# Kernel tuning notes

Measured on AMD Instinct MI355X. Metric: run time of the kernel, lower is better.

## Reference

```python
import jax, jax.numpy as jnp
import numpy as np

B, ID, OD = 4096, 2048, 1024


def _conv_softmax(x, w):
    # x: [..., L]; torch Conv1d(1,1,k=3,stride=1,pad=1,bias=False) then softmax(dim=-1)
    L = x.shape[-1]
    xp = jnp.pad(x, [(0, 0)] * (x.ndim - 1) + [(1, 1)])
    y = w[0] * xp[..., 0:L] + w[1] * xp[..., 1:L + 1] + w[2] * xp[..., 2:L + 2]
    return jax.nn.softmax(y, axis=-1)


def _lstm_cell(x, h, c, Wih, Whh, bih, bhh):
    # torch LSTMCell gate order: i, f, g, o
    g = x @ Wih.T + h @ Whh.T + (bih + bhh)
    i, f, gg, o = jnp.split(g, 4, axis=-1)
    c2 = jax.nn.sigmoid(f) * c + jax.nn.sigmoid(i) * jnp.tanh(gg)
    h2 = jax.nn.sigmoid(o) * jnp.tanh(c2)
    return h2, c2


def _lstm_params(key, in_dim, hid):
    k = 1.0 / np.sqrt(hid)
    ks = jax.random.split(key, 4)
    Wih = jax.random.uniform(ks[0], (4 * hid, in_dim), jnp.float32, -k, k)
    Whh = jax.random.uniform(ks[1], (4 * hid, hid), jnp.float32, -k, k)
    bih = jax.random.uniform(ks[2], (4 * hid,), jnp.float32, -k, k)
    bhh = jax.random.uniform(ks[3], (4 * hid,), jnp.float32, -k, k)
    return Wih, Whh, bih, bhh


def setup_inputs() -> dict:
    key = jax.random.key(0)
    ks = jax.random.split(key, 12)
    spec = jax.random.normal(ks[0], (B, ID), jnp.float32)
    Wih1, Whh1, bih1, bhh1 = _lstm_params(ks[1], ID, OD)
    Wih2, Whh2, bih2, bhh2 = _lstm_params(ks[2], ID // 2, OD // 2)
    Wih3, Whh3, bih3, bhh3 = _lstm_params(ks[3], ID // 4, OD // 4)
    Wih4, Whh4, bih4, bhh4 = _lstm_params(ks[4], ID // 8, OD // 8)
    ck = np.sqrt(1.0 / 3.0)  # Conv1d(1,1,3) init bound
    w2_1h = jax.random.uniform(ks[5], (3,), jnp.float32, -ck, ck)
    w2_1c = jax.random.uniform(ks[6], (3,), jnp.float32, -ck, ck)
    w3_2h = jax.random.uniform(ks[7], (3,), jnp.float32, -ck, ck)
    w3_2c = jax.random.uniform(ks[8], (3,), jnp.float32, -ck, ck)
    w4_3h = jax.random.uniform(ks[9], (3,), jnp.float32, -ck, ck)
    w4_3c = jax.random.uniform(ks[10], (3,), jnp.float32, -ck, ck)
    return dict(spec=spec,
                Wih1=Wih1, Whh1=Whh1, bih1=bih1, bhh1=bhh1,
                Wih2=Wih2, Whh2=Whh2, bih2=bih2, bhh2=bhh2,
                Wih3=Wih3, Whh3=Whh3, bih3=bih3, bhh3=bhh3,
                Wih4=Wih4, Whh4=Whh4, bih4=bih4, bhh4=bhh4,
                w2_1h=w2_1h, w2_1c=w2_1c, w3_2h=w3_2h, w3_2c=w3_2c,
                w4_3h=w4_3h, w4_3c=w4_3c)


def reference(spec, Wih1, Whh1, bih1, bhh1, Wih2, Whh2, bih2, bhh2,
              Wih3, Whh3, bih3, bhh3, Wih4, Whh4, bih4, bhh4,
              w2_1h, w2_1c, w3_2h, w3_2c, w4_3h, w4_3c):
    b = spec.shape[0]
    # Level 4: 8 independent steps, fresh zero state each (torch code passes no hidden)
    x4 = spec.reshape(b, 8, ID // 8)
    z4 = jnp.zeros((b, 8, OD // 8), spec.dtype)
    h4, c4 = _lstm_cell(x4, z4, z4, Wih4, Whh4, bih4, bhh4)   # [b,8,OD/8]
    hb4 = _conv_softmax(h4.reshape(b, 4, OD // 4), w4_3h)      # pairs -> [b,4,OD/4]
    cb4 = _conv_softmax(c4.reshape(b, 4, OD // 4), w4_3c)
    # Level 3: 4 independent steps seeded by level-4 blended states
    x3 = spec.reshape(b, 4, ID // 4)
    h3, c3 = _lstm_cell(x3, hb4, cb4, Wih3, Whh3, bih3, bhh3)  # [b,4,OD/4]
    hb3 = _conv_softmax(h3.reshape(b, 2, OD // 2), w3_2h)      # [b,2,OD/2]
    cb3 = _conv_softmax(c3.reshape(b, 2, OD // 2), w3_2c)
    # Level 2: 2 independent steps
    x2 = spec.reshape(b, 2, ID // 2)
    h2, c2 = _lstm_cell(x2, hb3, cb3, Wih2, Whh2, bih2, bhh2)  # [b,2,OD/2]
    hb2 = _conv_softmax(h2.reshape(b, OD), w2_1h)              # [b,OD]
    cb2 = _conv_softmax(c2.reshape(b, OD), w2_1c)
    # Level 1: single full-resolution step; forward returns out1 = h1
    h1, c1 = _lstm_cell(spec, hb2, cb2, Wih1, Whh1, bih1, bhh1)
    return h1
```

## Files before the change

kernel.cpp:

```cpp
#include <hip/hip_runtime.h>


typedef __bf16 bf16x8 __attribute__((ext_vector_type(8)));
typedef float f32x4 __attribute__((ext_vector_type(4)));
typedef unsigned short u16x4 __attribute__((ext_vector_type(4)));

#define AS1 __attribute__((address_space(1)))
#define AS3 __attribute__((address_space(3)))

__device__ __forceinline__ unsigned short f2bf(float f) {
    union { float f; unsigned int i; } v; v.f = f;
    unsigned int r = v.i + 0x7fffu + ((v.i >> 16) & 1u);
    return (unsigned short)(r >> 16);
}
__device__ __forceinline__ float bf2f(unsigned short u) {
    union { unsigned int i; float f; } v; v.i = ((unsigned int)u) << 16; return v.f;
}
__device__ __forceinline__ float sigm(float x) { return 1.f / (1.f + __expf(-x)); }
__device__ __forceinline__ float tanh_(float x) { float e = __expf(2.f * x); return 1.f - 2.f / (e + 1.f); }

__global__ __launch_bounds__(256) void cvt_spec3(
    const float* __restrict__ spec, unsigned short* __restrict__ sB,
    unsigned short* __restrict__ X, unsigned short* __restrict__ Y, long n4)
{
    const long stride = (long)gridDim.x * blockDim.x;
    for (long i = (long)blockIdx.x * blockDim.x + threadIdx.x; i < n4; i += stride) {
        const float4 v = ((const float4*)spec)[i];
        u16x4 o; o.x = f2bf(v.x); o.y = f2bf(v.y); o.z = f2bf(v.z); o.w = f2bf(v.w);
        ((u16x4*)sB)[i] = o;
        const long b = i >> 9;
        const int c4 = (int)(i & 511);
        *(u16x4*)(X + (b * 4 + (c4 >> 7)) * 768  + ((c4 & 127) << 2)) = o;
        *(u16x4*)(Y + (b * 2 + (c4 >> 8)) * 1536 + ((c4 & 255) << 2)) = o;
    }
}

__global__ __launch_bounds__(256) void cvt_specA(
    const float* __restrict__ spec, unsigned short* __restrict__ dst, long n4)
{
    const long stride = (long)gridDim.x * blockDim.x;
    for (long i = (long)blockIdx.x * blockDim.x + threadIdx.x; i < n4; i += stride) {
        const float4 v = ((const float4*)spec)[i];
        const long m = i >> 9;
        const int col = ((int)(i & 511)) << 2;
        u16x4 o; o.x = f2bf(v.x); o.y = f2bf(v.y); o.z = f2bf(v.z); o.w = f2bf(v.w);
        *(u16x4*)(dst + m * 3072 + col) = o;
    }
}

struct PSeg { const float* src; unsigned short* dst; long g0; int H; int kshift; int dstld; int dstcol; };
struct PArgs { PSeg s[7]; long total; };

__global__ __launch_bounds__(256) void cvt_permW_all(PArgs pa)
{
    const long stride = (long)gridDim.x * blockDim.x;
    for (long gi = (long)blockIdx.x * blockDim.x + threadIdx.x; gi < pa.total; gi += stride) {
        int si = 0;
#pragma unroll
        for (int k = 1; k < 7; ++k) si += (gi >= pa.s[k].g0);
        const PSeg sg = pa.s[si];
        const long i = gi - sg.g0;
        const int kq = 1 << sg.kshift;
        const int p = (int)(i >> sg.kshift);
        const int kk = ((int)i & (kq - 1)) << 2;
        const int o = ((p >> 6) << 4) | (p & 15);
        const int q = (p >> 4) & 3;
        const long r = (long)q * sg.H + o;
        const float4 v = *(const float4*)(sg.src + (r << (sg.kshift + 2)) + kk);
        u16x4 wv; wv.x = f2bf(v.x); wv.y = f2bf(v.y); wv.z = f2bf(v.z); wv.w = f2bf(v.w);
        *(u16x4*)(sg.dst + (long)p * sg.dstld + sg.dstcol + kk) = wv;
    }
}

__global__ __launch_bounds__(256) void bias_all(
    const float* __restrict__ bih1, const float* __restrict__ bhh1,
    const float* __restrict__ bih2, const float* __restrict__ bhh2,
    const float* __restrict__ bih3, const float* __restrict__ bhh3,
    const float* __restrict__ bih4, const float* __restrict__ bhh4,
    float* __restrict__ bs1, float* __restrict__ bs2,
    float* __restrict__ bs3, float* __restrict__ bs4)
{
    const int i = blockIdx.x * 256 + threadIdx.x;
    const float *bih, *bhh; float* dst; int H, j;
    if (i < 4096)      { bih = bih1; bhh = bhh1; dst = bs1; H = 1024; j = i; }
    else if (i < 6144) { bih = bih2; bhh = bhh2; dst = bs2; H = 512;  j = i - 4096; }
    else if (i < 7168) { bih = bih3; bhh = bhh3; dst = bs3; H = 256;  j = i - 6144; }
    else               { bih = bih4; bhh = bhh4; dst = bs4; H = 128;  j = i - 7168; }
    const int o = ((j >> 6) << 4) | (j & 15);
    const int q = (j >> 4) & 3;
    dst[j] = bih[q * H + o] + bhh[q * H + o];
}

#define QUAD(AF, S, NS, BF)                                                                 \
    { _Pragma("unroll") for (int mi = 0; mi < 4; ++mi) {                                    \
        _Pragma("unroll") for (int ni = 0; ni < 2; ++ni) {                                  \
            acc[(S)*4+mi][(NS)*2+ni] = __builtin_amdgcn_mfma_f32_16x16x32_bf16(             \
                AF[mi][0], BF[ni][0], acc[(S)*4+mi][(NS)*2+ni], 0, 0, 0);                   \
            acc[(S)*4+mi][(NS)*2+ni] = __builtin_amdgcn_mfma_f32_16x16x32_bf16(             \
                AF[mi][1], BF[ni][1], acc[(S)*4+mi][(NS)*2+ni], 0, 0, 0);                   \
    } } }

#define GLL(gsrc, loff) __builtin_amdgcn_global_load_lds(                                   \
    (const AS1 void*)(gsrc), (AS3 void*)(lds + (loff)), 16, 0, 0)

#define FENCE asm volatile("" ::: "memory")

template<bool HAS_CIN, bool LAST>
__global__ __launch_bounds__(512, 2) void gemm8(
    const unsigned short* __restrict__ A, const unsigned short* __restrict__ W, const int K,
    const float* __restrict__ bsum, const unsigned short* __restrict__ Cin,
    float* __restrict__ HoutF, unsigned short* __restrict__ HoutB,
    unsigned short* __restrict__ CoutB, const int H)
{
    __shared__ __align__(16) char lds[131072];
    const int t = threadIdx.x;
    const int w = t >> 6, l = t & 63;
    const int wr = w >> 2, wc = w & 3;

    const int GX = gridDim.x, GY = gridDim.y;
    const int nwg = GX * GY;
    const int bid = (int)blockIdx.y * GX + (int)blockIdx.x;
    const int swz = (bid & 7) * (nwg >> 3) + (bid >> 3);
    const int m0 = (swz / GY) * 256, n0 = (swz % GY) * 256;

    const int colsw = ((l & 7) ^ (l >> 3)) * 8;
    const size_t k128 = (size_t)128 * K;
    const size_t aoff0 = (size_t)(m0 + w * 16 + (l >> 3)) * K + colsw;
    const size_t aoff1 = aoff0 + (size_t)8 * K;
    const size_t boff0 = (size_t)(n0 + w * 16 + (l >> 3)) * K + colsw;
    const size_t boff1 = boff0 + (size_t)8 * K;
    const int sd0 = w * 2048 + l * 16;
    const int sd1 = sd0 + 1024;

    const int lr128 = (l & 15) * 128;
    const int sw0 = (((l >> 4)    ) ^ (l & 7)) * 16;
    const int sw1 = (((l >> 4) + 4) ^ (l & 7)) * 16;

    f32x4 acc[8][4];
#pragma unroll
    for (int i = 0; i < 8; ++i)
#pragma unroll
        for (int j = 0; j < 4; ++j) acc[i][j] = (f32x4){0.f, 0.f, 0.f, 0.f};

    const int NT = K >> 6;

    GLL(A + aoff0, sd0);                      GLL(A + aoff1, sd1);
    GLL(A + aoff0 + k128, 16384 + sd0);       GLL(A + aoff1 + k128, 16384 + sd1);
    GLL(W + boff0, 32768 + sd0);              GLL(W + boff1, 32768 + sd1);
    GLL(W + boff0 + k128, 49152 + sd0);       GLL(W + boff1 + k128, 49152 + sd1);
    GLL(W + boff0 + 64, 98304 + sd0);         GLL(W + boff1 + 64, 98304 + sd1);
    GLL(W + boff0 + k128 + 64, 114688 + sd0); GLL(W + boff1 + k128 + 64, 114688 + sd1);

    bf16x8 aLo[4][2], aHi[4][2], bF0[2][2], bF1[2][2];

    for (int tt = 0; tt < NT; ++tt) {
        const int q = tt & 1, qn = q ^ 1;
        const int rbA = (q << 16) + (wr << 14) + lr128;
        const int rbB = (q << 16) + 32768 + wc * 8192 + lr128;
        const bool st1 = (tt + 1 < NT), st2 = (tt + 2 < NT);

        if (st1) { asm volatile("s_waitcnt vmcnt(4)" ::: "memory"); }
        else     { asm volatile("s_waitcnt vmcnt(0)" ::: "memory"); }
        __builtin_amdgcn_s_barrier();
        FENCE;

#pragma unroll
        for (int mi = 0; mi < 4; ++mi) {
            aLo[mi][0] = *(const bf16x8*)(lds + rbA + mi * 2048 + sw0);
            aLo[mi][1] = *(const bf16x8*)(lds + rbA + mi * 2048 + sw1);
        }
#pragma unroll
        for (int ni = 0; ni < 2; ++ni) {
            bF0[ni][0] = *(const bf16x8*)(lds + rbB + ni * 2048 + sw0);
            bF0[ni][1] = *(const bf16x8*)(lds + rbB + ni * 2048 + sw1);
            bF1[ni][0] = *(const bf16x8*)(lds + rbB + 4096 + ni * 2048 + sw0);
            bF1[ni][1] = *(const bf16x8*)(lds + rbB + 4096 + ni * 2048 + sw1);
        }
        if (st1) {
            const size_t ko1 = (size_t)(tt + 1) * 64;
            GLL(A + aoff0 + ko1, (qn << 16) + sd0);
            GLL(A + aoff1 + ko1, (qn << 16) + sd1);
            GLL(A + aoff0 + k128 + ko1, (qn << 16) + 16384 + sd0);
            GLL(A + aoff1 + k128 + ko1, (qn << 16) + 16384 + sd1);
        }
#pragma unroll
        for (int mi = 0; mi < 4; ++mi) {
            aHi[mi][0] = *(const bf16x8*)(lds + rbA + 8192 + mi * 2048 + sw0);
            aHi[mi][1] = *(const bf16x8*)(lds + rbA + 8192 + mi * 2048 + sw1);
        }

        __builtin_amdgcn_s_setprio(1);
        QUAD(aLo, 0, 0, bF0);
        QUAD(aLo, 0, 1, bF1);
        __builtin_amdgcn_s_setprio(0);
        __builtin_amdgcn_s_barrier();
        FENCE;

        if (st2) {
            const size_t ko2 = (size_t)(tt + 2) * 64;
            GLL(W + boff0 + ko2, (q << 16) + 32768 + sd0);
            GLL(W + boff1 + ko2, (q << 16) + 32768 + sd1);
            GLL(W + boff0 + k128 + ko2, (q << 16) + 49152 + sd0);
            GLL(W + boff1 + k128 + ko2, (q << 16) + 49152 + sd1);
        }
        __builtin_amdgcn_s_setprio(1);
        QUAD(aHi, 1, 1, bF1);
        QUAD(aHi, 1, 0, bF0);
        __builtin_amdgcn_s_setprio(0);
    }

    const int ocol = (n0 >> 6) * 16 + wc * 16 + (l & 15);
    const int bb = n0 + wc * 64 + (l & 15);
    const float b0 = bsum[bb], b1 = bsum[bb + 16], b2 = bsum[bb + 32], b3 = bsum[bb + 48];
    const int mrow0 = m0 + wr * 128 + (l >> 4) * 4;
#pragma unroll
    for (int mi = 0; mi < 8; ++mi)
#pragma unroll
        for (int j = 0; j < 4; ++j) {
            const size_t m = (size_t)(mrow0 + mi * 16 + j);
            const float gi = acc[mi][0][j] + b0;
            const float gf = acc[mi][1][j] + b1;
            const float gg = acc[mi][2][j] + b2;
            const float go = acc[mi][3][j] + b3;
            float c2 = sigm(gi) * tanh_(gg);
            if (HAS_CIN) c2 += sigm(gf) * bf2f(Cin[m * H + ocol]);
            const float h2 = sigm(go) * tanh_(c2);
            if (LAST) {
                HoutF[m * H + ocol] = h2;
            } else {
                HoutB[m * H + ocol] = f2bf(h2);
                CoutB[m * H + ocol] = f2bf(c2);
            }
        }
}

template<int L>
__global__ __launch_bounds__(256) void conv_dual(
    const unsigned short* __restrict__ Hin, const unsigned short* __restrict__ Cin,
    const float* __restrict__ w3h, const float* __restrict__ w3c,
    unsigned short* __restrict__ Yb, int ldYb, unsigned short* __restrict__ cbuf)
{
    __shared__ float xs[L + 2];
    __shared__ float red[8];
    const int nrows = gridDim.x >> 1;
    const bool isC = (int)blockIdx.x >= nrows;
    const int row = isC ? ((int)blockIdx.x - nrows) : (int)blockIdx.x;
    const unsigned short* Xs = isC ? Cin : Hin;
    const float* w3 = isC ? w3c : w3h;
    const int t = threadIdx.x;
    const size_t base = (size_t)row * L;
    const float w0 = w3[0], w1 = w3[1], w2 = w3[2];
    if (t == 0) { xs[0] = 0.f; xs[L + 1] = 0.f; }
    for (int i = t; i < L; i += 256) xs[i + 1] = bf2f(Xs[base + i]);
    __syncthreads();
    constexpr int E = L / 256;
    float y[E];
    float vmax = -3.4e38f;
#pragma unroll
    for (int i = 0; i < E; ++i) {
        const int c = t + i * 256;
        y[i] = w0 * xs[c] + w1 * xs[c + 1] + w2 * xs[c + 2];
        vmax = fmaxf(vmax, y[i]);
    }
#pragma unroll
    for (int off = 32; off >= 1; off >>= 1) vmax = fmaxf(vmax, __shfl_xor(vmax, off));
    if ((t & 63) == 0) red[t >> 6] = vmax;
    __syncthreads();
    vmax = fmaxf(fmaxf(red[0], red[1]), fmaxf(red[2], red[3]));
    float s = 0.f;
#pragma unroll
    for (int i = 0; i < E; ++i) { y[i] = __expf(y[i] - vmax); s += y[i]; }
#pragma unroll
    for (int off = 32; off >= 1; off >>= 1) s += __shfl_xor(s, off);
    if ((t & 63) == 0) red[4 + (t >> 6)] = s;
    __syncthreads();
    const float inv = 1.f / (red[4] + red[5] + red[6] + red[7]);
#pragma unroll
    for (int i = 0; i < E; ++i) {
        const int c = t + i * 256;
        const float v = y[i] * inv;
        if (isC) cbuf[base + c] = f2bf(v);
        else     Yb[(size_t)row * ldYb + c] = f2bf(v);
    }
}

extern "C" void kernel_launch(void* const* d_in, const int* in_sizes, int n_in,
                              void* d_out, int out_size, void* d_ws, size_t ws_size,
                              hipStream_t stream)
{
    (void)in_sizes; (void)n_in; (void)out_size; (void)ws_size;
    const float* spec  = (const float*)d_in[0];
    const float* Wih1  = (const float*)d_in[1];
    const float* Whh1  = (const float*)d_in[2];
    const float* bih1  = (const float*)d_in[3];
    const float* bhh1  = (const float*)d_in[4];
    const float* Wih2  = (const float*)d_in[5];
    const float* Whh2  = (const float*)d_in[6];
    const float* bih2  = (const float*)d_in[7];
    const float* bhh2  = (const float*)d_in[8];
    const float* Wih3  = (const float*)d_in[9];
    const float* Whh3  = (const float*)d_in[10];
    const float* bih3  = (const float*)d_in[11];
    const float* bhh3  = (const float*)d_in[12];
    const float* Wih4  = (const float*)d_in[13];
    const float* bih4  = (const float*)d_in[15];
    const float* bhh4  = (const float*)d_in[16];
    const float* w2_1h = (const float*)d_in[17];
    const float* w2_1c = (const float*)d_in[18];
    const float* w3_2h = (const float*)d_in[19];
    const float* w3_2c = (const float*)d_in[20];
    const float* w4_3h = (const float*)d_in[21];
    const float* w4_3c = (const float*)d_in[22];

    char* ws = (char*)d_ws;
    unsigned short* h   = (unsigned short*)(ws + 0);
    unsigned short* c   = (unsigned short*)(ws + (size_t)8388608);
    unsigned short* cb  = (unsigned short*)(ws + (size_t)16777216);
    unsigned short* sB  = (unsigned short*)(ws + (size_t)25165824);
    unsigned short* X   = (unsigned short*)(ws + (size_t)41943040);
    unsigned short* Y   = (unsigned short*)(ws + (size_t)67108864);
    unsigned short* Wc1 = (unsigned short*)(ws + (size_t)92274688);
    unsigned short* Wc2 = (unsigned short*)(ws + (size_t)117440512);
    unsigned short* Wc3 = (unsigned short*)(ws + (size_t)123731968);
    unsigned short* W4  = (unsigned short*)(ws + (size_t)125304832);
    float*          bs1 = (float*)(ws + (size_t)125566976);
    float*          bs2 = bs1 + 4096;
    float*          bs3 = bs2 + 4096;
    float*          bs4 = bs3 + 4096;

    cvt_spec3<<<2048, 256, 0, stream>>>(spec, sB, X, Y, 2097152);
    PArgs pa;
    pa.s[0] = { Wih1, Wc1,       0, 1024, 9, 3072,    0 };
    pa.s[1] = { Whh1, Wc1, 2097152, 1024, 8, 3072, 2048 };
    pa.s[2] = { Wih2, Wc2, 3145728,  512, 8, 1536,    0 };
    pa.s[3] = { Whh2, Wc2, 3670016,  512, 7, 1536, 1024 };
    pa.s[4] = { Wih3, Wc3, 3932160,  256, 7,  768,    0 };
    pa.s[5] = { Whh3, Wc3, 4063232,  256, 6,  768,  512 };
    pa.s[6] = { Wih4, W4,  4128768,  128, 6,  256,    0 };
    pa.total = 4161536;
    cvt_permW_all<<<2048, 256, 0, stream>>>(pa);
    bias_all<<<30, 256, 0, stream>>>(bih1, bhh1, bih2, bhh2, bih3, bhh3, bih4, bhh4,
                                     bs1, bs2, bs3, bs4);

    gemm8<false, false><<<dim3(128, 2), 512, 0, stream>>>(sB, W4, 256, bs4, nullptr,
                                                          nullptr, h, c, 128);
    conv_dual<256><<<32768, 256, 0, stream>>>(h, c, w4_3h, w4_3c, X + 512, 768, cb);

    gemm8<true, false><<<dim3(64, 4), 512, 0, stream>>>(X, Wc3, 768, bs3, cb,
                                                        nullptr, h, c, 256);
    cvt_specA<<<2048, 256, 0, stream>>>(spec, X, 2097152);
    conv_dual<512><<<16384, 256, 0, stream>>>(h, c, w3_2h, w3_2c, Y + 1024, 1536, cb);

    gemm8<true, false><<<dim3(32, 8), 512, 0, stream>>>(Y, Wc2, 1536, bs2, cb,
                                                        nullptr, h, c, 512);
    conv_dual<1024><<<8192, 256, 0, stream>>>(h, c, w2_1h, w2_1c, X + 2048, 3072, cb);

    gemm8<true, true><<<dim3(16, 16), 512, 0, stream>>>(X, Wc1, 3072, bs1, cb,
                                                        (float*)d_out, nullptr, nullptr, 1024);
}
```

Measured before the change: 307.6 us.

## Pack multiple rows per conv-softmax block and drop separate spec re-conversion

The conv+softmax kernel now handles 2048 elements per block: several short rows per block with 16-byte vectorized loads and stores, and sub-wavefront shuffle reductions in place of block-wide syncs for the smaller rows. This cuts the block count and the per-element scalar memory traffic. The level-1 input spec is now written once, in the first conversion kernel, into a new buffer Z rather than re-converted by a separate kernel mid-pipeline. That removes one launch and one extra read of spec, at the cost of more workspace.

```diff
diff --git a/kernel.cpp b/kernel.cpp
--- a/kernel.cpp
+++ b/kernel.cpp
@@ -4,6 +4,7 @@
 typedef __bf16 bf16x8 __attribute__((ext_vector_type(8)));
 typedef float f32x4 __attribute__((ext_vector_type(4)));
 typedef unsigned short u16x4 __attribute__((ext_vector_type(4)));
+typedef unsigned short u16x8 __attribute__((ext_vector_type(8)));
 
 #define AS1 __attribute__((address_space(1)))
 #define AS3 __attribute__((address_space(3)))
@@ -19,9 +20,10 @@
 __device__ __forceinline__ float sigm(float x) { return 1.f / (1.f + __expf(-x)); }
 __device__ __forceinline__ float tanh_(float x) { float e = __expf(2.f * x); return 1.f - 2.f / (e + 1.f); }
 
-__global__ __launch_bounds__(256) void cvt_spec3(
+__global__ __launch_bounds__(256) void cvt_spec4(
     const float* __restrict__ spec, unsigned short* __restrict__ sB,
-    unsigned short* __restrict__ X, unsigned short* __restrict__ Y, long n4)
+    unsigned short* __restrict__ X, unsigned short* __restrict__ Y,
+    unsigned short* __restrict__ Z, long n4)
 {
     const long stride = (long)gridDim.x * blockDim.x;
     for (long i = (long)blockIdx.x * blockDim.x + threadIdx.x; i < n4; i += stride) {
@@ -32,19 +34,7 @@
         const int c4 = (int)(i & 511);
         *(u16x4*)(X + (b * 4 + (c4 >> 7)) * 768  + ((c4 & 127) << 2)) = o;
         *(u16x4*)(Y + (b * 2 + (c4 >> 8)) * 1536 + ((c4 & 255) << 2)) = o;
-    }
-}
-
-__global__ __launch_bounds__(256) void cvt_specA(
-    const float* __restrict__ spec, unsigned short* __restrict__ dst, long n4)
-{
-    const long stride = (long)gridDim.x * blockDim.x;
-    for (long i = (long)blockIdx.x * blockDim.x + threadIdx.x; i < n4; i += stride) {
-        const float4 v = ((const float4*)spec)[i];
-        const long m = i >> 9;
-        const int col = ((int)(i & 511)) << 2;
-        u16x4 o; o.x = f2bf(v.x); o.y = f2bf(v.y); o.z = f2bf(v.z); o.w = f2bf(v.w);
-        *(u16x4*)(dst + m * 3072 + col) = o;
+        *(u16x4*)(Z + b * 3072 + (c4 << 2)) = o;
     }
 }
 
@@ -240,48 +230,58 @@
     const float* __restrict__ w3h, const float* __restrict__ w3c,
     unsigned short* __restrict__ Yb, int ldYb, unsigned short* __restrict__ cbuf)
 {
-    __shared__ float xs[L + 2];
+    constexpr int R = 2048 / L;
+    constexpr int TPR = L / 8;
+    __shared__ float xs[R][L + 2];
     __shared__ float red[8];
-    const int nrows = gridDim.x >> 1;
-    const bool isC = (int)blockIdx.x >= nrows;
-    const int row = isC ? ((int)blockIdx.x - nrows) : (int)blockIdx.x;
+    const int nb = gridDim.x >> 1;
+    const bool isC = (int)blockIdx.x >= nb;
+    const int row0 = (isC ? (int)blockIdx.x - nb : (int)blockIdx.x) * R;
     const unsigned short* Xs = isC ? Cin : Hin;
     const float* w3 = isC ? w3c : w3h;
     const int t = threadIdx.x;
-    const size_t base = (size_t)row * L;
+    const int r = t / TPR;
+    const int c8 = (t % TPR) * 8;
     const float w0 = w3[0], w1 = w3[1], w2 = w3[2];
-    if (t == 0) { xs[0] = 0.f; xs[L + 1] = 0.f; }
-    for (int i = t; i < L; i += 256) xs[i + 1] = bf2f(Xs[base + i]);
+
+    const u16x8 v = *(const u16x8*)(Xs + (size_t)(row0 + r) * L + c8);
+#pragma unroll
+    for (int k = 0; k < 8; ++k) xs[r][c8 + 1 + k] = bf2f(v[k]);
+    if (t < R) { xs[t][0] = 0.f; xs[t][L + 1] = 0.f; }
     __syncthreads();
-    constexpr int E = L / 256;
-    float y[E];
+
+    float y[8];
     float vmax = -3.4e38f;
 #pragma unroll
-    for (int i = 0; i < E; ++i) {
-        const int c = t + i * 256;
-        y[i] = w0 * xs[c] + w1 * xs[c + 1] + w2 * xs[c + 2];
-        vmax = fmaxf(vmax, y[i]);
-    }
-#pragma unroll
-    for (int off = 32; off >= 1; off >>= 1) vmax = fmaxf(vmax, __shfl_xor(vmax, off));
-    if ((t & 63) == 0) red[t >> 6] = vmax;
-    __syncthreads();
-    vmax = fmaxf(fmaxf(red[0], red[1]), fmaxf(red[2], red[3]));
+    for (int k = 0; k < 8; ++k) {
+        y[k] = w0 * xs[r][c8 + k] + w1 * xs[r][c8 + k + 1] + w2 * xs[r][c8 + k + 2];
+        vmax = fmaxf(vmax, y[k]);
+    }
+#pragma unroll
+    for (int off = (TPR >= 64 ? 32 : TPR / 2); off >= 1; off >>= 1)
+        vmax = fmaxf(vmax, __shfl_xor(vmax, off));
+    if (TPR == 128) {
+        if ((t & 63) == 0) red[t >> 6] = vmax;
+        __syncthreads();
+        vmax = fmaxf(red[2 * r], red[2 * r + 1]);
+    }
     float s = 0.f;
 #pragma unroll
-    for (int i = 0; i < E; ++i) { y[i] = __expf(y[i] - vmax); s += y[i]; }
-#pragma unroll
-    for (int off = 32; off >= 1; off >>= 1) s += __shfl_xor(s, off);
-    if ((t & 63) == 0) red[4 + (t >> 6)] = s;
-    __syncthreads();
-    const float inv = 1.f / (red[4] + red[5] + red[6] + red[7]);
-#pragma unroll
-    for (int i = 0; i < E; ++i) {
-        const int c = t + i * 256;
-        const float v = y[i] * inv;
-        if (isC) cbuf[base + c] = f2bf(v);
-        else     Yb[(size_t)row * ldYb + c] = f2bf(v);
-    }
+    for (int k = 0; k < 8; ++k) { y[k] = __expf(y[k] - vmax); s += y[k]; }
+#pragma unroll
+    for (int off = (TPR >= 64 ? 32 : TPR / 2); off >= 1; off >>= 1)
+        s += __shfl_xor(s, off);
+    if (TPR == 128) {
+        if ((t & 63) == 0) red[4 + (t >> 6)] = s;
+        __syncthreads();
+        s = red[4 + 2 * r] + red[4 + 2 * r + 1];
+    }
+    const float inv = 1.f / s;
+    u16x8 o;
+#pragma unroll
+    for (int k = 0; k < 8; ++k) o[k] = f2bf(y[k] * inv);
+    if (isC) *(u16x8*)(cbuf + (size_t)(row0 + r) * L + c8) = o;
+    else     *(u16x8*)(Yb + (size_t)(row0 + r) * ldYb + c8) = o;
 }
 
 extern "C" void kernel_launch(void* const* d_in, const int* in_sizes, int n_in,
@@ -319,16 +319,17 @@
     unsigned short* sB  = (unsigned short*)(ws + (size_t)25165824);
     unsigned short* X   = (unsigned short*)(ws + (size_t)41943040);
     unsigned short* Y   = (unsigned short*)(ws + (size_t)67108864);
-    unsigned short* Wc1 = (unsigned short*)(ws + (size_t)92274688);
-    unsigned short* Wc2 = (unsigned short*)(ws + (size_t)117440512);
-    unsigned short* Wc3 = (unsigned short*)(ws + (size_t)123731968);
-    unsigned short* W4  = (unsigned short*)(ws + (size_t)125304832);
-    float*          bs1 = (float*)(ws + (size_t)125566976);
+    unsigned short* Z   = (unsigned short*)(ws + (size_t)92274688);
+    unsigned short* Wc1 = (unsigned short*)(ws + (size_t)117440512);
+    unsigned short* Wc2 = (unsigned short*)(ws + (size_t)142606336);
+    unsigned short* Wc3 = (unsigned short*)(ws + (size_t)148897792);
+    unsigned short* W4  = (unsigned short*)(ws + (size_t)150470656);
+    float*          bs1 = (float*)(ws + (size_t)150732800);
     float*          bs2 = bs1 + 4096;
     float*          bs3 = bs2 + 4096;
     float*          bs4 = bs3 + 4096;
 
-    cvt_spec3<<<2048, 256, 0, stream>>>(spec, sB, X, Y, 2097152);
+    cvt_spec4<<<2048, 256, 0, stream>>>(spec, sB, X, Y, Z, 2097152);
     PArgs pa;
     pa.s[0] = { Wih1, Wc1,       0, 1024, 9, 3072,    0 };
     pa.s[1] = { Whh1, Wc1, 2097152, 1024, 8, 3072, 2048 };
@@ -344,17 +345,16 @@
 
     gemm8<false, false><<<dim3(128, 2), 512, 0, stream>>>(sB, W4, 256, bs4, nullptr,
                                                           nullptr, h, c, 128);
-    conv_dual<256><<<32768, 256, 0, stream>>>(h, c, w4_3h, w4_3c, X + 512, 768, cb);
+    conv_dual<256><<<4096, 256, 0, stream>>>(h, c, w4_3h, w4_3c, X + 512, 768, cb);
 
     gemm8<true, false><<<dim3(64, 4), 512, 0, stream>>>(X, Wc3, 768, bs3, cb,
                                                         nullptr, h, c, 256);
-    cvt_specA<<<2048, 256, 0, stream>>>(spec, X, 2097152);
-    conv_dual<512><<<16384, 256, 0, stream>>>(h, c, w3_2h, w3_2c, Y + 1024, 1536, cb);
+    conv_dual<512><<<4096, 256, 0, stream>>>(h, c, w3_2h, w3_2c, Y + 1024, 1536, cb);
 
     gemm8<true, false><<<dim3(32, 8), 512, 0, stream>>>(Y, Wc2, 1536, bs2, cb,
                                                         nullptr, h, c, 512);
-    conv_dual<1024><<<8192, 256, 0, stream>>>(h, c, w2_1h, w2_1c, X + 2048, 3072, cb);
-
-    gemm8<true, true><<<dim3(16, 16), 512, 0, stream>>>(X, Wc1, 3072, bs1, cb,
+    conv_dual<1024><<<4096, 256, 0, stream>>>(h, c, w2_1h, w2_1c, Z + 2048, 3072, cb);
+
+    gemm8<true, true><<<dim3(16, 16), 512, 0, stream>>>(Z, Wc1, 3072, bs1, cb,
                                                         (float*)d_out, nullptr, nullptr, 1024);
 }
```

Measured after the change: 277.8 us. -9.7%, faster.
